# Kernel tuning notes

Measured on AMD Instinct MI355X. Metric: run time of the kernel, lower is better.

## Reference

```python
import jax, jax.numpy as jnp
import numpy as np

NUM_NODES = 50000
NUM_RELS = 256
D = 256            # node_in_feat
TEXT_D = 256       # text_emb_dim
T_TOTAL = 24       # number of unique timestep graphs
E = 20000          # edges per timestep graph
B = 16             # batch of query times
SEQ_LEN = 7


def setup_inputs() -> dict:
    key = jax.random.key(0)
    ks = jax.random.split(key, 12)
    s = 1.0 / np.sqrt(D)
    return {
        "node_embeds": jax.random.normal(ks[0], (NUM_NODES, D), jnp.float32),
        "text_emb": jax.random.normal(ks[1], (T_TOTAL, E, TEXT_D), jnp.float32),
        "text_w_W": jax.random.uniform(ks[2], (TEXT_D, D), jnp.float32, -s, s),
        "text_w_b": jax.random.uniform(ks[3], (D,), jnp.float32, -s, s),
        "edge_w_W": jax.random.uniform(ks[4], (3 * D, D), jnp.float32, -s, s),
        "edge_w_b": jax.random.uniform(ks[5], (D,), jnp.float32, -s, s),
        "gru_Wih": jax.random.uniform(ks[6], (D, 3 * D), jnp.float32, -s, s),
        "gru_Whh": jax.random.uniform(ks[7], (D, 3 * D), jnp.float32, -s, s),
        "gru_bih": jax.random.uniform(ks[8], (3 * D,), jnp.float32, -s, s),
        "gru_bhh": jax.random.uniform(ks[9], (3 * D,), jnp.float32, -s, s),
        "edge_src": jax.random.randint(ks[10], (T_TOTAL, E), 0, NUM_NODES, jnp.int32),
        "edge_dst": jax.random.randint(jax.random.fold_in(ks[10], 1), (T_TOTAL, E), 0, NUM_NODES, jnp.int32),
        "edge_rel": jax.random.randint(jax.random.fold_in(ks[10], 2), (T_TOTAL, E), 0, NUM_RELS, jnp.int32),
        "time_idx": jax.random.randint(ks[11], (B, SEQ_LEN), 0, T_TOTAL, jnp.int32),
    }


def _gru(seqs, Wih, Whh, bih, bhh):
    # seqs: [B, R, S, d] -> run GRU over S, return final hidden [B, R, d]
    xs = jnp.moveaxis(seqs, 2, 0)  # [S, B, R, d]
    h0 = jnp.zeros(seqs.shape[:2] + (seqs.shape[-1],), seqs.dtype)

    def step(h, x):
        gi = x @ Wih + bih            # [B, R, 3d]
        gh = h @ Whh + bhh
        i_r, i_z, i_n = jnp.split(gi, 3, axis=-1)
        h_r, h_z, h_n = jnp.split(gh, 3, axis=-1)
        r = jax.nn.sigmoid(i_r + h_r)
        z = jax.nn.sigmoid(i_z + h_z)
        n = jnp.tanh(i_n + r * h_n)
        h_new = (1.0 - z) * n + z * h
        return h_new, None

    h_final, _ = jax.lax.scan(step, h0, xs)
    return h_final


def reference(node_embeds, text_emb, text_w_W, text_w_b, edge_w_W, edge_w_b,
              gru_Wih, gru_Whh, gru_bih, gru_bhh,
              edge_src, edge_dst, edge_rel, time_idx):
    # edge text projection (text_w): [T, E, D]
    text_h = text_emb @ text_w_W + text_w_b
    # gather node embeddings per edge endpoint
    h_src = node_embeds[edge_src]  # [T, E, D]
    h_dst = node_embeds[edge_dst]  # [T, E, D]
    # concat + edge MLP + ReLU: e_h = relu(edge_w([src || text || dst]))
    e = jnp.concatenate([h_src, text_h, h_dst], axis=-1)  # [T, E, 3D]
    e_h = jax.nn.relu(e @ edge_w_W + edge_w_b)            # [T, E, D]

    # scatter-mean of edge embeddings by relation type per timestep graph;
    # relations absent in a graph get zeros (init_rel_embeds = zeros)
    seg = lambda v, r: jax.ops.segment_sum(v, r, num_segments=NUM_RELS)
    sums = jax.vmap(seg)(e_h, edge_rel)                               # [T, R, D]
    counts = jax.vmap(seg)(jnp.ones(edge_rel.shape, e_h.dtype), edge_rel)  # [T, R]
    counts = counts[..., None]
    rel_emb = jnp.where(counts > 0, sums / jnp.maximum(counts, 1.0), 0.0)  # [T, R, D]

    # per query time: gather its window of timestep rel-embeddings and run
    # the GRU over time (relations act as the GRU batch dim, like transpose(0,1))
    seqs = rel_emb[time_idx]                 # [B, S, R, D]
    seqs = jnp.swapaxes(seqs, 1, 2)          # [B, R, S, D]
    hn = _gru(seqs, gru_Wih, gru_Whh, gru_bih, gru_bhh)  # [B, R, D]
    return hn
```

## Files before the change

### kernel.cpp

```cpp
#include <hip/hip_runtime.h>
#include <cstdint>
#include <cstddef>

#define NNODES 50000
#define NPAD   50048
#define NRELS  256
#define DIM    256
#define TT     24
#define EE     20000
#define BATCH  16
#define SEQQ   7

typedef __bf16 bf16;
typedef __bf16 bf16x4 __attribute__((ext_vector_type(4)));
typedef __bf16 bf16x8 __attribute__((ext_vector_type(8)));
typedef float  f32x4  __attribute__((ext_vector_type(4)));

__device__ __forceinline__ void gload16(const void* g, void* l){
  __builtin_amdgcn_global_load_lds((const __attribute__((address_space(1))) void*)g,
                                   (__attribute__((address_space(3))) void*)l, 16, 0, 0);
}


__global__ void k_cvt8(const float* __restrict__ in, bf16* __restrict__ out, int n8){
  int i = blockIdx.x*256 + threadIdx.x;
  if (i >= n8) return;
  const float4* p = (const float4*)in + (size_t)i*2;
  float4 a = p[0], b = p[1];
  bf16x8 o;
  o[0]=(bf16)a.x; o[1]=(bf16)a.y; o[2]=(bf16)a.z; o[3]=(bf16)a.w;
  o[4]=(bf16)b.x; o[5]=(bf16)b.y; o[6]=(bf16)b.z; o[7]=(bf16)b.w;
  ((bf16x8*)out)[i] = o;
}

__global__ void k_build_wbt(const float* __restrict__ tW, const float* __restrict__ eW,
                            bf16* __restrict__ WbT){
  int n = blockIdx.x, j = threadIdx.x;
  WbT[(size_t)n*768 + j]       = (bf16)eW[(size_t)j*256 + n];
  WbT[(size_t)n*768 + 512 + j] = (bf16)eW[(size_t)(512+j)*256 + n];
  float acc = 0.f;
  for (int m=0; m<256; ++m) acc += tW[(size_t)j*256 + m] * eW[(size_t)(256+m)*256 + n];
  WbT[(size_t)n*768 + 256 + j] = (bf16)acc;
}

__global__ void k_bias(const float* __restrict__ tb, const float* __restrict__ eW,
                       const float* __restrict__ eb, float* __restrict__ bf){
  int n = threadIdx.x;
  float acc = eb[n];
  for (int m=0; m<256; ++m) acc += tb[m] * eW[(size_t)(256+m)*256 + n];
  bf[n] = acc;
}

__global__ void k_gruWT(const float* __restrict__ W, bf16* __restrict__ WT){
  int n = blockIdx.x, k = threadIdx.x;
  WT[(size_t)n*256 + k] = (bf16)W[(size_t)k*768 + n];
}

__global__ void k_hist(const int* __restrict__ rel, int* __restrict__ counts,
                       int* __restrict__ offs, int* __restrict__ cursor){
  __shared__ int hist[256];
  __shared__ int scan[256];
  int t = blockIdx.x, tid = threadIdx.x;
  hist[tid] = 0;
  __syncthreads();
  for (int e = tid; e < EE; e += 256) atomicAdd(&hist[rel[(size_t)t*EE + e]], 1);
  __syncthreads();
  int v = hist[tid];
  scan[tid] = v;
  __syncthreads();
  for (int d=1; d<256; d<<=1){
    int add = (tid >= d) ? scan[tid-d] : 0;
    __syncthreads();
    scan[tid] += add;
    __syncthreads();
  }
  int ex = scan[tid] - v;
  counts[t*256+tid] = v;
  offs[t*256+tid]   = ex;
  cursor[t*256+tid] = ex;
}

__global__ void k_perm(const int* __restrict__ rel, const int* __restrict__ esrc,
                       const int* __restrict__ edst, int* __restrict__ cursor,
                       int* __restrict__ gperm, int* __restrict__ src_p,
                       int* __restrict__ dst_p, int* __restrict__ tr_p){
  int t = blockIdx.y;
  int e = blockIdx.x*256 + threadIdx.x;
  if (e < EE){
    int r = rel[(size_t)t*EE + e];
    int p = atomicAdd(&cursor[t*256 + r], 1);
    size_t g = (size_t)t*EE + p;
    gperm[g] = t*EE + e;
    src_p[g] = esrc[(size_t)t*EE + e];
    dst_p[g] = edst[(size_t)t*EE + e];
    tr_p[g]  = t*256 + r;
  }
}

__global__ __launch_bounds__(256) void k_projn(
    const bf16* __restrict__ Abf, const bf16* __restrict__ WbT, int koff,
    bf16* __restrict__ out)
{
  int m0 = blockIdx.x*128;
  int tid = threadIdx.x, lane = tid&63, w = tid>>6;
  int l15 = lane&15, lq = lane>>4;
  int c0 = w*64;
  __shared__ __align__(16) bf16 Al[128*32];
  __shared__ __align__(16) bf16 Bl[256*32];

  f32x4 acc[8][4];
  f32x4 z4 = {0.f,0.f,0.f,0.f};
  #pragma unroll
  for (int mi=0;mi<8;++mi)
    #pragma unroll
    for (int ni=0;ni<4;++ni) acc[mi][ni]=z4;

  for (int ks=0; ks<8; ++ks){
    int k0 = ks*32;
    #pragma unroll
    for (int p=0;p<2;++p){
      int c = p*256 + tid;
      int rw = c>>2, prt = c&3;
      int pp = prt ^ ((rw>>1)&3);
      const char* src = (const char*)(Abf + (size_t)(m0+rw)*256 + k0) + pp*16;
      gload16(src, (char*)Al + (size_t)(p*256 + w*64)*16);
    }
    #pragma unroll
    for (int p=0;p<4;++p){
      int c = p*256 + tid;
      int nn = c>>2, prt = c&3;
      int pp = prt ^ ((nn>>1)&3);
      const char* src = (const char*)(WbT + (size_t)nn*768 + koff + k0) + pp*16;
      gload16(src, (char*)Bl + (size_t)(p*256 + w*64)*16);
    }
    __syncthreads();
    bf16x8 b[4];
    #pragma unroll
    for (int ni=0;ni<4;++ni){
      int nn = c0 + ni*16 + l15;
      b[ni] = *(const bf16x8*)((const char*)Bl + (size_t)nn*64 + (size_t)((lq ^ ((nn>>1)&3))*16));
    }
    #pragma unroll
    for (int mi=0;mi<8;++mi){
      int rw = mi*16 + l15;
      bf16x8 a = *(const bf16x8*)((const char*)Al + (size_t)rw*64 + (size_t)((lq ^ ((rw>>1)&3))*16));
      #pragma unroll
      for (int ni=0;ni<4;++ni)
        acc[mi][ni] = __builtin_amdgcn_mfma_f32_16x16x32_bf16(b[ni], a, acc[mi][ni], 0,0,0);
    }
    __syncthreads();
  }
  #pragma unroll
  for (int mi=0;mi<8;++mi){
    int row = m0 + mi*16 + l15;
    #pragma unroll
    for (int ni=0;ni<4;++ni){
      bf16x4 o;
      #pragma unroll
      for (int q=0;q<4;++q) o[q] = (bf16)acc[mi][ni][q];
      *(bf16x4*)(out + (size_t)row*256 + c0 + ni*16 + lq*4) = o;
    }
  }
}

__global__ __launch_bounds__(256,3) void k_projtc(
    const float* __restrict__ text, const int* __restrict__ gperm,
    const bf16* __restrict__ WbT, const float* __restrict__ bfused,
    const bf16* __restrict__ P, const bf16* __restrict__ Q,
    const int* __restrict__ src_p, const int* __restrict__ dst_p,
    const int* __restrict__ tr_p, float* __restrict__ rel_sum)
{
  int m0 = blockIdx.x*64;
  int tid = threadIdx.x, lane = tid&63, w = tid>>6;
  int l15 = lane&15, lq = lane>>4;
  int c0 = w*64;
  __shared__ __align__(16) float Afl[2][64*32];
  __shared__ __align__(16) bf16  Bl[2][256*32];
  __shared__ int trA[64], sIl[64], dIl[64];
  __shared__ int runS[65], runT[64];
  __shared__ int nRunS;

  if (tid < 64){
    int g = m0 + tid;
    trA[tid] = tr_p[g];
    sIl[tid] = src_p[g];
    dIl[tid] = dst_p[g];
  }
  __syncthreads();
  if (tid == 0){
    int nR = 0;
    for (int i=0;i<64;++i){
      if (i==0 || trA[i]!=trA[i-1]){ runS[nR]=i; runT[nR]=trA[i]; ++nR; }
    }
    runS[nR] = 64;
    nRunS = nR;
  }

  int rA0 = tid>>3;
  int partA = tid&7;
  int ppA = partA ^ (rA0 & 7);
  const float* aPtr0 = text + (size_t)gperm[m0 + rA0]*256      + ppA*4;
  const float* aPtr1 = text + (size_t)gperm[m0 + 32 + rA0]*256 + ppA*4;

#define STAGEA(KS, BI)                                                        \
  { gload16(aPtr0 + (KS)*32, (char*)&Afl[BI][0] + (size_t)(w*64)*16);         \
    gload16(aPtr1 + (KS)*32, (char*)&Afl[BI][0] + (size_t)(256 + w*64)*16); }

#define STAGEB(KS, BI)                                                        \
  { _Pragma("unroll")                                                         \
    for (int p_=0;p_<4;++p_){                                                 \
      int c_ = p_*256 + tid;                                                  \
      int nn_ = c_>>2, prt_ = c_&3;                                           \
      int pp_ = prt_ ^ ((nn_>>1)&3);                                          \
      const char* src_ = (const char*)(WbT + (size_t)nn_*768 + 256 + (KS)*32) + pp_*16; \
      gload16(src_, (char*)&Bl[BI][0] + (size_t)(p_*256 + w*64)*16); } }

  f32x4 acc[4][4];
  f32x4 z4 = {0.f,0.f,0.f,0.f};
  #pragma unroll
  for (int mi=0;mi<4;++mi)
    #pragma unroll
    for (int ni=0;ni<4;++ni) acc[mi][ni]=z4;

  STAGEA(0, 0);
  STAGEB(0, 0);

  #pragma unroll
  for (int ks=0; ks<8; ++ks){
    const int bi = ks & 1;
    if (ks < 7){
      STAGEA(ks+1, bi^1);
      STAGEB(ks+1, bi^1);
      asm volatile("s_waitcnt vmcnt(6)\n\ts_barrier" ::: "memory");
    } else {
      asm volatile("s_waitcnt vmcnt(0)\n\ts_barrier" ::: "memory");
    }
    __builtin_amdgcn_sched_barrier(0);
    bf16x8 a[4], b[4];
    #pragma unroll
    for (int ni=0;ni<4;++ni){
      int nn = c0 + ni*16 + l15;
      b[ni] = *(const bf16x8*)((const char*)&Bl[bi][0]
               + (size_t)nn*64 + (size_t)((lq ^ ((nn>>1)&3))*16));
    }
    #pragma unroll
    for (int mi=0;mi<4;++mi){
      int rw = mi*16 + l15;
      int sw = l15 & 7;
      const char* ab = (const char*)&Afl[bi][0] + (size_t)rw*128;
      f32x4 f0 = *(const f32x4*)(ab + (size_t)(((lq*2+0)^sw))*16);
      f32x4 f1 = *(const f32x4*)(ab + (size_t)(((lq*2+1)^sw))*16);
      bf16x8 o;
      o[0]=(bf16)f0[0]; o[1]=(bf16)f0[1]; o[2]=(bf16)f0[2]; o[3]=(bf16)f0[3];
      o[4]=(bf16)f1[0]; o[5]=(bf16)f1[1]; o[6]=(bf16)f1[2]; o[7]=(bf16)f1[3];
      a[mi] = o;
    }
    asm volatile("s_waitcnt lgkmcnt(0)" ::: "memory");
    __builtin_amdgcn_sched_barrier(0);
    #pragma unroll
    for (int mi=0;mi<4;++mi)
      #pragma unroll
      for (int ni=0;ni<4;++ni)
        acc[mi][ni] = __builtin_amdgcn_mfma_f32_16x16x32_bf16(b[ni], a[mi], acc[mi][ni], 0,0,0);
    if (ks < 7)
      __builtin_amdgcn_s_barrier();
  }
#undef STAGEA
#undef STAGEB

  float4 bias4[4];
  #pragma unroll
  for (int ni=0;ni<4;++ni)
    bias4[ni] = *(const float4*)(bfused + c0 + ni*16 + lq*4);

  #pragma unroll
  for (int mi=0;mi<4;++mi){
    int row = mi*16 + l15;
    int srow = sIl[row], drow = dIl[row];
    #pragma unroll
    for (int ni=0;ni<4;++ni){
      bf16x4 pv = *(const bf16x4*)(P + (size_t)srow*256 + c0 + ni*16 + lq*4);
      bf16x4 qv = *(const bf16x4*)(Q + (size_t)drow*256 + c0 + ni*16 + lq*4);
      f32x4 t4 = acc[mi][ni];
      t4[0] = fmaxf(t4[0] + (float)pv[0] + (float)qv[0] + bias4[ni].x, 0.f);
      t4[1] = fmaxf(t4[1] + (float)pv[1] + (float)qv[1] + bias4[ni].y, 0.f);
      t4[2] = fmaxf(t4[2] + (float)pv[2] + (float)qv[2] + bias4[ni].z, 0.f);
      t4[3] = fmaxf(t4[3] + (float)pv[3] + (float)qv[3] + bias4[ni].w, 0.f);
      acc[mi][ni] = t4;
    }
  }

  int nR = nRunS;
  for (int k=0; k<nR; ++k){
    int rs = runS[k], re = runS[k+1], tr = runT[k];
    float part16[16];
    #pragma unroll
    for (int ni=0;ni<4;++ni){
      #pragma unroll
      for (int q=0;q<4;++q){
        float s = 0.f;
        #pragma unroll
        for (int mi=0;mi<4;++mi){
          int row = mi*16 + l15;
          s += (row >= rs && row < re) ? acc[mi][ni][q] : 0.f;
        }
        part16[ni*4+q] = s;
      }
    }
    #pragma unroll
    for (int m=1; m<16; m<<=1){
      #pragma unroll
      for (int s=0;s<16;++s) part16[s] += __shfl_xor(part16[s], m);
    }
    float v = part16[0];
    #pragma unroll
    for (int s=1;s<16;++s) v = (l15==s) ? part16[s] : v;
    atomicAdd(&rel_sum[(size_t)tr*256 + c0 + ((l15>>2)<<4) + (lq<<2) + (l15&3)], v);
  }
}

__global__ void k_mean(const float* __restrict__ rel_sum, const int* __restrict__ counts,
                       bf16* __restrict__ rel_bf){
  int tr = blockIdx.x, c = threadIdx.x;
  int cnt = counts[tr];
  float v = (cnt > 0) ? rel_sum[(size_t)tr*256 + c] / (float)cnt : 0.f;
  rel_bf[(size_t)tr*256 + c] = (bf16)v;
}

__global__ __launch_bounds__(256) void k_gemm(
    const bf16* __restrict__ A, const bf16* __restrict__ BT,
    const float* __restrict__ bias, float* __restrict__ Out)
{
  int m0 = blockIdx.x*128, n0 = blockIdx.y*128;
  int tid = threadIdx.x, lane = tid&63, w = tid>>6;
  int l15 = lane&15, lq = lane>>4;
  __shared__ __align__(16) bf16 Al[128*32];
  __shared__ __align__(16) bf16 Bl[128*32];
  int wr = (w&1)*64, wc = (w>>1)*64;
  f32x4 acc[4][4];
  f32x4 z4 = {0.f,0.f,0.f,0.f};
  #pragma unroll
  for (int mi=0;mi<4;++mi)
    #pragma unroll
    for (int ni=0;ni<4;++ni) acc[mi][ni]=z4;
  for (int ks=0; ks<8; ++ks){
    int k0 = ks*32;
    #pragma unroll
    for (int p=0;p<2;++p){
      int c = p*256 + tid;
      int rw = c>>2, part = c&3;
      int pp = part ^ ((rw>>1)&3);
      const char* src = (const char*)(A + (size_t)(m0+rw)*256 + k0) + pp*16;
      gload16(src, (char*)Al + (size_t)(p*256 + w*64)*16);
    }
    #pragma unroll
    for (int p=0;p<2;++p){
      int c = p*256 + tid;
      int nn = c>>2, part = c&3;
      int pp = part ^ ((nn>>1)&3);
      const char* src = (const char*)(BT + (size_t)(n0+nn)*256 + k0) + pp*16;
      gload16(src, (char*)Bl + (size_t)(p*256 + w*64)*16);
    }
    __syncthreads();
    bf16x8 a[4], b[4];
    #pragma unroll
    for (int mi=0;mi<4;++mi){
      int rw = wr + mi*16 + l15;
      a[mi] = *(const bf16x8*)((const char*)Al + (size_t)rw*64 + (size_t)((lq ^ ((rw>>1)&3))*16));
    }
    #pragma unroll
    for (int ni=0;ni<4;++ni){
      int nn = wc + ni*16 + l15;
      b[ni] = *(const bf16x8*)((const char*)Bl + (size_t)nn*64 + (size_t)((lq ^ ((nn>>1)&3))*16));
    }
    #pragma unroll
    for (int mi=0;mi<4;++mi)
      #pragma unroll
      for (int ni=0;ni<4;++ni)
        acc[mi][ni] = __builtin_amdgcn_mfma_f32_16x16x32_bf16(a[mi], b[ni], acc[mi][ni], 0,0,0);
    __syncthreads();
  }
  #pragma unroll
  for (int ni=0;ni<4;++ni){
    int col = n0 + wc + ni*16 + l15;
    float bv = bias[col];
    #pragma unroll
    for (int mi=0;mi<4;++mi){
      #pragma unroll
      for (int q=0;q<4;++q){
        int row = m0 + wr + mi*16 + lq*4 + q;
        Out[(size_t)row*768 + col] = acc[mi][ni][q] + bv;
      }
    }
  }
}

__global__ __launch_bounds__(256) void k_gru(
    const float* __restrict__ GI, const bf16* __restrict__ WhhT,
    const float* __restrict__ bhh, const int* __restrict__ time_idx,
    float* __restrict__ out)
{
  int blk = blockIdx.x;
  int tid = threadIdx.x, lane = tid&63, w = tid>>6;
  int l15 = lane&15, lq = lane>>4;
  int b = blk >> 4;
  int rr = ((blk & 15)*16) + l15;
  __shared__ __align__(16) bf16 Ah[16*256];

  f32x4 h[4];
  #pragma unroll
  for (int jq=0;jq<4;++jq) h[jq] = f32x4{0.f,0.f,0.f,0.f};

  for (int s=0; s<SEQQ; ++s){
    int t = time_idx[b*SEQQ + s];
    size_t gib = (size_t)(t*256 + rr)*768;
    f32x4 gh[12];
    #pragma unroll
    for (int ni=0;ni<12;++ni){
      int col = (ni>>2)*256 + w*64 + (ni&3)*16 + lq*4;
      gh[ni] = *(const f32x4*)(bhh + col);
    }
    if (s > 0){
      #pragma unroll
      for (int ks=0; ks<8; ++ks){
        bf16x8 a = *(const bf16x8*)(&Ah[0] + (size_t)l15*256 + ks*32 + lq*8);
        #pragma unroll
        for (int ni=0;ni<12;++ni){
          int n = (ni>>2)*256 + w*64 + (ni&3)*16 + l15;
          bf16x8 wv = *(const bf16x8*)(WhhT + (size_t)n*256 + ks*32 + lq*8);
          gh[ni] = __builtin_amdgcn_mfma_f32_16x16x32_bf16(wv, a, gh[ni], 0,0,0);
        }
      }
    }
    #pragma unroll
    for (int jq=0;jq<4;++jq){
      int col = w*64 + jq*16 + lq*4;
      f32x4 ir = *(const f32x4*)(GI + gib + col);
      f32x4 iz = *(const f32x4*)(GI + gib + 256 + col);
      f32x4 in = *(const f32x4*)(GI + gib + 512 + col);
      #pragma unroll
      for (int q=0;q<4;++q){
        float rg = 1.f/(1.f + __expf(-(ir[q] + gh[jq][q])));
        float zz = 1.f/(1.f + __expf(-(iz[q] + gh[4+jq][q])));
        float nn = tanhf(in[q] + rg*gh[8+jq][q]);
        h[jq][q] = (1.f - zz)*nn + zz*h[jq][q];
      }
    }
    if (s < SEQQ-1){
      __syncthreads();
      #pragma unroll
      for (int jq=0;jq<4;++jq){
        bf16x4 o;
        #pragma unroll
        for (int q=0;q<4;++q) o[q] = (bf16)h[jq][q];
        *(bf16x4*)(&Ah[0] + (size_t)l15*256 + w*64 + jq*16 + lq*4) = o;
      }
      __syncthreads();
    }
  }
  #pragma unroll
  for (int jq=0;jq<4;++jq){
    f32x4 o = h[jq];
    *(f32x4*)(out + (size_t)(blk*16 + l15)*256 + w*64 + jq*16 + lq*4) = o;
  }
}

extern "C" void kernel_launch(void* const* d_in, const int* in_sizes, int n_in,
                              void* d_out, int out_size, void* d_ws, size_t ws_size,
                              hipStream_t stream)
{
  (void)in_sizes; (void)n_in; (void)out_size; (void)ws_size;
  const float* node_embeds = (const float*)d_in[0];
  const float* text_emb    = (const float*)d_in[1];
  const float* text_w_W    = (const float*)d_in[2];
  const float* text_w_b    = (const float*)d_in[3];
  const float* edge_w_W    = (const float*)d_in[4];
  const float* edge_w_b    = (const float*)d_in[5];
  const float* gru_Wih     = (const float*)d_in[6];
  const float* gru_Whh     = (const float*)d_in[7];
  const float* gru_bih     = (const float*)d_in[8];
  const float* gru_bhh     = (const float*)d_in[9];
  const int* edge_src      = (const int*)d_in[10];
  const int* edge_dst      = (const int*)d_in[11];
  const int* edge_rel      = (const int*)d_in[12];
  const int* time_idx      = (const int*)d_in[13];
  float* out = (float*)d_out;
  char* ws = (char*)d_ws;

  size_t o = 0;
  bf16*  WbT    = (bf16*) (ws + o); o += (size_t)768*256*2;
  bf16*  WihT   = (bf16*) (ws + o); o += (size_t)768*256*2;
  bf16*  WhhT   = (bf16*) (ws + o); o += (size_t)768*256*2;
  float* bfused = (float*)(ws + o); o += 1024;
  bf16*  node_bf= (bf16*) (ws + o); o += (size_t)NPAD*256*2;
  int*   counts = (int*)  (ws + o); o += (size_t)TT*256*4;
  int*   offs   = (int*)  (ws + o); o += (size_t)TT*256*4;
  int*   cursor = (int*)  (ws + o); o += (size_t)TT*256*4;
  int*   gperm  = (int*)  (ws + o); o += (size_t)TT*EE*4;
  int*   src_p  = (int*)  (ws + o); o += (size_t)TT*EE*4;
  int*   dst_p  = (int*)  (ws + o); o += (size_t)TT*EE*4;
  int*   tr_p   = (int*)  (ws + o); o += (size_t)TT*EE*4;
  bf16*  rel_bf = (bf16*) (ws + o); o += (size_t)TT*256*256*2;
  bf16*  P      = (bf16*) (ws + o); o += (size_t)NPAD*256*2;
  bf16*  Q      = (bf16*) (ws + o); o += (size_t)NPAD*256*2;
  float* rel_sum= (float*)(ws + o); o += (size_t)TT*256*256*4;
  float* GI     = (float*)(ws + o); o += (size_t)TT*256*768*4;

  k_cvt8<<<6250,256,0,stream>>>(node_embeds, node_bf, NNODES*256/8);
  k_build_wbt<<<256,256,0,stream>>>(text_w_W, edge_w_W, WbT);
  k_bias<<<1,256,0,stream>>>(text_w_b, edge_w_W, edge_w_b, bfused);
  k_gruWT<<<768,256,0,stream>>>(gru_Wih, WihT);
  k_gruWT<<<768,256,0,stream>>>(gru_Whh, WhhT);
  k_hist<<<TT,256,0,stream>>>(edge_rel, counts, offs, cursor);
  k_perm<<<dim3((EE+255)/256,TT),256,0,stream>>>(edge_rel, edge_src, edge_dst,
                                                 cursor, gperm, src_p, dst_p, tr_p);
  k_projn<<<NPAD/128,256,0,stream>>>(node_bf, WbT, 0,   P);
  k_projn<<<NPAD/128,256,0,stream>>>(node_bf, WbT, 512, Q);
  hipMemsetAsync(rel_sum, 0, (size_t)TT*256*256*4, stream);
  k_projtc<<<TT*EE/64,256,0,stream>>>(text_emb, gperm, WbT, bfused, P, Q,
                                      src_p, dst_p, tr_p, rel_sum);
  k_mean<<<TT*256,256,0,stream>>>(rel_sum, counts, rel_bf);
  k_gemm<<<dim3(48,6),256,0,stream>>>(rel_bf, WihT, gru_bih, GI);
  k_gru<<<256,256,0,stream>>>(GI, WhhT, gru_bhh, time_idx, out);
}
```

Measured before the change: 540.1 us.

## Load weight fragments directly to registers and triple-buffer text tiles in LDS

The projection GEMM kernel stops staging the weight B-tile through shared memory. Each wave now loads its bf16x8 fragments straight from global memory into double-buffered registers. The text A-tile moves from two to three LDS buffers with prefetch distance two, and the vmcnt waits are retuned to match. This removes the LDS writes and reads for B, cuts LDS footprint, and deepens the A prefetch. In exchange it adds register pressure and issues uncoalesced direct global loads for B that depend on cache hits, and the hand-counted vmcnt values must be exact for correctness.

```diff
diff --git a/kernel.cpp b/kernel.cpp
--- a/kernel.cpp
+++ b/kernel.cpp
@@ -174,8 +174,7 @@
   int tid = threadIdx.x, lane = tid&63, w = tid>>6;
   int l15 = lane&15, lq = lane>>4;
   int c0 = w*64;
-  __shared__ __align__(16) float Afl[2][64*32];
-  __shared__ __align__(16) bf16  Bl[2][256*32];
+  __shared__ __align__(16) float Afl[3][64*32];
   __shared__ int trA[64], sIl[64], dIl[64];
   __shared__ int runS[65], runT[64];
   __shared__ int nRunS;
@@ -202,18 +201,16 @@
   const float* aPtr0 = text + (size_t)gperm[m0 + rA0]*256      + ppA*4;
   const float* aPtr1 = text + (size_t)gperm[m0 + 32 + rA0]*256 + ppA*4;
 
+  const bf16* bBase = WbT + (size_t)(c0 + l15)*768 + 256 + lq*8;
+
 #define STAGEA(KS, BI)                                                        \
   { gload16(aPtr0 + (KS)*32, (char*)&Afl[BI][0] + (size_t)(w*64)*16);         \
     gload16(aPtr1 + (KS)*32, (char*)&Afl[BI][0] + (size_t)(256 + w*64)*16); }
 
-#define STAGEB(KS, BI)                                                        \
+#define LOADB(KS, DST)                                                        \
   { _Pragma("unroll")                                                         \
-    for (int p_=0;p_<4;++p_){                                                 \
-      int c_ = p_*256 + tid;                                                  \
-      int nn_ = c_>>2, prt_ = c_&3;                                           \
-      int pp_ = prt_ ^ ((nn_>>1)&3);                                          \
-      const char* src_ = (const char*)(WbT + (size_t)nn_*768 + 256 + (KS)*32) + pp_*16; \
-      gload16(src_, (char*)&Bl[BI][0] + (size_t)(p_*256 + w*64)*16); } }
+    for (int ni_=0;ni_<4;++ni_)                                               \
+      DST[ni_] = *(const bf16x8*)(bBase + (size_t)ni_*16*768 + (KS)*32); }
 
   f32x4 acc[4][4];
   f32x4 z4 = {0.f,0.f,0.f,0.f};
@@ -222,32 +219,31 @@
     #pragma unroll
     for (int ni=0;ni<4;++ni) acc[mi][ni]=z4;
 
+  bf16x8 bA[4], bB[4];
   STAGEA(0, 0);
-  STAGEB(0, 0);
+  LOADB(0, bA);
+  STAGEA(1, 1);
 
   #pragma unroll
   for (int ks=0; ks<8; ++ks){
-    const int bi = ks & 1;
     if (ks < 7){
-      STAGEA(ks+1, bi^1);
-      STAGEB(ks+1, bi^1);
-      asm volatile("s_waitcnt vmcnt(6)\n\ts_barrier" ::: "memory");
+      if ((ks & 1) == 0){ LOADB(ks+1, bB); } else { LOADB(ks+1, bA); }
+    }
+    if (ks < 6) STAGEA(ks+2, (ks+2)%3);
+    if (ks < 6){
+      asm volatile("s_waitcnt vmcnt(12)\n\ts_barrier" ::: "memory");
+    } else if (ks == 6){
+      asm volatile("s_waitcnt vmcnt(10)\n\ts_barrier" ::: "memory");
     } else {
-      asm volatile("s_waitcnt vmcnt(0)\n\ts_barrier" ::: "memory");
+      asm volatile("s_waitcnt vmcnt(4)\n\ts_barrier" ::: "memory");
     }
     __builtin_amdgcn_sched_barrier(0);
-    bf16x8 a[4], b[4];
-    #pragma unroll
-    for (int ni=0;ni<4;++ni){
-      int nn = c0 + ni*16 + l15;
-      b[ni] = *(const bf16x8*)((const char*)&Bl[bi][0]
-               + (size_t)nn*64 + (size_t)((lq ^ ((nn>>1)&3))*16));
-    }
+    bf16x8 a[4];
     #pragma unroll
     for (int mi=0;mi<4;++mi){
       int rw = mi*16 + l15;
       int sw = l15 & 7;
-      const char* ab = (const char*)&Afl[bi][0] + (size_t)rw*128;
+      const char* ab = (const char*)&Afl[ks%3][0] + (size_t)rw*128;
       f32x4 f0 = *(const f32x4*)(ab + (size_t)(((lq*2+0)^sw))*16);
       f32x4 f1 = *(const f32x4*)(ab + (size_t)(((lq*2+1)^sw))*16);
       bf16x8 o;
@@ -257,16 +253,24 @@
     }
     asm volatile("s_waitcnt lgkmcnt(0)" ::: "memory");
     __builtin_amdgcn_sched_barrier(0);
-    #pragma unroll
-    for (int mi=0;mi<4;++mi)
-      #pragma unroll
-      for (int ni=0;ni<4;++ni)
-        acc[mi][ni] = __builtin_amdgcn_mfma_f32_16x16x32_bf16(b[ni], a[mi], acc[mi][ni], 0,0,0);
+    if ((ks & 1) == 0){
+      #pragma unroll
+      for (int mi=0;mi<4;++mi)
+        #pragma unroll
+        for (int ni=0;ni<4;++ni)
+          acc[mi][ni] = __builtin_amdgcn_mfma_f32_16x16x32_bf16(bA[ni], a[mi], acc[mi][ni], 0,0,0);
+    } else {
+      #pragma unroll
+      for (int mi=0;mi<4;++mi)
+        #pragma unroll
+        for (int ni=0;ni<4;++ni)
+          acc[mi][ni] = __builtin_amdgcn_mfma_f32_16x16x32_bf16(bB[ni], a[mi], acc[mi][ni], 0,0,0);
+    }
     if (ks < 7)
       __builtin_amdgcn_s_barrier();
   }
 #undef STAGEA
-#undef STAGEB
+#undef LOADB
 
   float4 bias4[4];
   #pragma unroll
```

Result: slower. 555.0 us (+2.7%).
